# Kernel tuning notes

Measured on AMD Instinct MI355X. Metric: run time of the kernel, lower is better.

## Reference

```python
import jax, jax.numpy as jnp
import numpy as np

B, T, P, L, H = 65536, 256, 4, 14, 32
IN = P + L  # 18


def setup_inputs() -> dict:
    key = jax.random.key(0)
    ks = jax.random.split(key, 8)
    s1 = 1.0 / np.sqrt(IN)
    s2 = 1.0 / np.sqrt(H)
    return {
        "phys": jax.random.normal(ks[0], (B, T, P), dtype=jnp.float32),
        "latents": jax.random.normal(ks[1], (B, L), dtype=jnp.float32),
        "W1": jax.random.uniform(ks[2], (IN, H), jnp.float32, -s1, s1),
        "b1": jax.random.uniform(ks[3], (H,), jnp.float32, -s1, s1),
        "W2": jax.random.uniform(ks[4], (H, H), jnp.float32, -s2, s2),
        "b2": jax.random.uniform(ks[5], (H,), jnp.float32, -s2, s2),
        "W3": jax.random.uniform(ks[6], (H, L), jnp.float32, -s2, s2),
        "b3": jax.random.uniform(ks[7], (L,), jnp.float32, -s2, s2),
    }


def reference(phys, latents, W1, b1, W2, b2, W3, b3):
    # phys: [B, T, P]; latents: [B, L]. Dropout p=0.0 -> identity (eval-equivalent).
    phys_t = jnp.swapaxes(phys, 0, 1)  # [T, B, P] for scan over time

    def step(lat, ph):
        x = jnp.concatenate([ph, lat], axis=1)          # [B, P+L]
        h = jax.nn.relu(x @ W1 + b1)                    # [B, H]
        h = jax.nn.relu(h @ W2 + b2)                    # [B, H]
        lat = lat + (h @ W3 + b3)                       # residual update [B, L]
        return lat, lat

    _, outs = jax.lax.scan(step, latents, phys_t)       # outs: [T, B, L]
    return jnp.swapaxes(outs, 0, 1)                     # [B, T, L]
```

## Files before the change

kernel.cpp:

```cpp
#include <hip/hip_runtime.h>


#define BB 65536
#define TT 256
#define LL 14
#define HH 32

typedef float f32x16 __attribute__((ext_vector_type(16)));
typedef __bf16 bf16x8 __attribute__((ext_vector_type(8)));
typedef __bf16 bf16x2 __attribute__((ext_vector_type(2)));
typedef int i32x2 __attribute__((ext_vector_type(2)));

static __device__ __forceinline__ unsigned packbf(float a, float b) {
    bf16x2 p;
    p[0] = (__bf16)a;
    p[1] = (__bf16)b;
    return __builtin_bit_cast(unsigned, p);
}

static __device__ __forceinline__ void split2(float v0, float v1,
                                              unsigned& hw, unsigned& lw) {
    const __bf16 h0 = (__bf16)v0, h1 = (__bf16)v1;
    hw = packbf(v0, v1);
    const float l0 = v0 - (float)h0;
    const float l1 = v1 - (float)h1;
    lw = packbf(l0, l1);
}

static __device__ __forceinline__ bf16x8 mkfrag(unsigned w0, unsigned w1,
                                                unsigned w2, unsigned w3) {
    union { unsigned u[4]; bf16x8 v; } x;
    x.u[0] = w0; x.u[1] = w1; x.u[2] = w2; x.u[3] = w3;
    return x.v;
}

static __device__ __forceinline__ f32x16 mf(bf16x8 a, bf16x8 b, f32x16 c) {
    return __builtin_amdgcn_mfma_f32_32x32x16_bf16(a, b, c, 0, 0, 0);
}

#if __has_builtin(__builtin_amdgcn_permlane32_swap)
static __device__ __forceinline__ void xswap(unsigned a, unsigned b,
                                             unsigned& a_out, unsigned& b_out) {
    i32x2 r = __builtin_amdgcn_permlane32_swap((int)a, (int)b, false, false);
    a_out = (unsigned)r[0];
    b_out = (unsigned)r[1];
}
#else
static __device__ __forceinline__ void xswap(unsigned a, unsigned b,
                                             unsigned& a_out, unsigned& b_out) {
    const int lane = threadIdx.x & 63;
    const int idx = (lane ^ 32) << 2;
    unsigned sa = (unsigned)__builtin_amdgcn_ds_bpermute(idx, (int)a);
    unsigned sb = (unsigned)__builtin_amdgcn_ds_bpermute(idx, (int)b);
    const bool hi = lane >= 32;
    a_out = hi ? sb : a;
    b_out = hi ? b : sa;
}
#endif

static __device__ __forceinline__ void hfrag(const f32x16& h,
                                             bf16x8& B0h, bf16x8& B0l,
                                             bf16x8& B1h, bf16x8& B1l) {
    unsigned Wh[8], Wl[8];
#pragma unroll
    for (int p = 0; p < 8; ++p) split2(h[2 * p], h[2 * p + 1], Wh[p], Wl[p]);
    unsigned a02h, b02h, a02l, b02l, a13h, b13h, a13l, b13l;
    xswap(Wh[0], Wh[2], a02h, b02h); xswap(Wl[0], Wl[2], a02l, b02l);
    xswap(Wh[1], Wh[3], a13h, b13h); xswap(Wl[1], Wl[3], a13l, b13l);
    B0h = mkfrag(a02h, a13h, b02h, b13h);
    B0l = mkfrag(a02l, a13l, b02l, b13l);
    unsigned a46h, b46h, a46l, b46l, a57h, b57h, a57l, b57l;
    xswap(Wh[4], Wh[6], a46h, b46h); xswap(Wl[4], Wl[6], a46l, b46l);
    xswap(Wh[5], Wh[7], a57h, b57h); xswap(Wl[5], Wl[7], a57l, b57l);
    B1h = mkfrag(a46h, a57h, b46h, b57h);
    B1l = mkfrag(a46l, a57l, b46l, b57l);
}

__global__ __launch_bounds__(256, 2)
void emulator_kernel(const float* __restrict__ phys,
                     const float* __restrict__ latents,
                     const float* __restrict__ W1g,
                     const float* __restrict__ b1g,
                     const float* __restrict__ W2g,
                     const float* __restrict__ b2g,
                     const float* __restrict__ W3g,
                     const float* __restrict__ b3g,
                     float* __restrict__ out) {
    const int tid = threadIdx.x;
    const int lane = tid & 63;
    const int wv = tid >> 6;
    const int c = lane & 31;
    const bool hi = lane >= 32;
    const int kb = hi ? 8 : 0;
    const int r = blockIdx.x * 128 + wv * 32 + c;

    bf16x8 A1t0h, A1t0l, A1c;
    {
        unsigned hw[4], lw[4];
#pragma unroll
        for (int w = 0; w < 4; ++w) {
            const int k0 = kb + 2 * w;
            split2(W1g[k0 * HH + c], W1g[(k0 + 1) * HH + c], hw[w], lw[w]);
        }
        A1t0h = mkfrag(hw[0], hw[1], hw[2], hw[3]);
        A1t0l = mkfrag(lw[0], lw[1], lw[2], lw[3]);
        unsigned whp, wlp;
        split2(W1g[16 * HH + c], W1g[17 * HH + c], whp, wlp);
        A1c = hi ? mkfrag(0, 0, 0, 0) : mkfrag(whp, whp, wlp, 0);
    }
    bf16x8 A2h0, A2l0, A2h1, A2l1, A3h0, A3l0, A3h1, A3l1;
    {
        unsigned hw[4], lw[4];
#pragma unroll
        for (int w = 0; w < 4; ++w) {
            const int k0 = kb + 2 * w;
            split2(W2g[k0 * HH + c], W2g[(k0 + 1) * HH + c], hw[w], lw[w]);
        }
        A2h0 = mkfrag(hw[0], hw[1], hw[2], hw[3]);
        A2l0 = mkfrag(lw[0], lw[1], lw[2], lw[3]);
#pragma unroll
        for (int w = 0; w < 4; ++w) {
            const int k0 = 16 + kb + 2 * w;
            split2(W2g[k0 * HH + c], W2g[(k0 + 1) * HH + c], hw[w], lw[w]);
        }
        A2h1 = mkfrag(hw[0], hw[1], hw[2], hw[3]);
        A2l1 = mkfrag(lw[0], lw[1], lw[2], lw[3]);
#pragma unroll
        for (int w = 0; w < 4; ++w) {
            const int k0 = kb + 2 * w;
            const float e0 = (c < LL) ? W3g[k0 * LL + c] : 0.0f;
            const float e1 = (c < LL) ? W3g[(k0 + 1) * LL + c] : 0.0f;
            split2(e0, e1, hw[w], lw[w]);
        }
        A3h0 = mkfrag(hw[0], hw[1], hw[2], hw[3]);
        A3l0 = mkfrag(lw[0], lw[1], lw[2], lw[3]);
#pragma unroll
        for (int w = 0; w < 4; ++w) {
            const int k0 = 16 + kb + 2 * w;
            const float e0 = (c < LL) ? W3g[k0 * LL + c] : 0.0f;
            const float e1 = (c < LL) ? W3g[(k0 + 1) * LL + c] : 0.0f;
            split2(e0, e1, hw[w], lw[w]);
        }
        A3h1 = mkfrag(hw[0], hw[1], hw[2], hw[3]);
        A3l1 = mkfrag(lw[0], lw[1], lw[2], lw[3]);
    }

    f32x16 cb1, cb2, cb3, z;
#pragma unroll
    for (int rr = 0; rr < 16; ++rr) {
        const int row = (rr & 3) + 8 * (rr >> 2) + (hi ? 4 : 0);
        cb1[rr] = b1g[row];
        cb2[rr] = b2g[row];
        cb3[rr] = (row < LL) ? b3g[row] : 0.0f;
        z[rr] = 0.0f;
    }

    f32x16 lat;
#pragma unroll
    for (int i = 0; i < 16; ++i) lat[i] = 0.0f;
    {
        const float* lrow = latents + (size_t)r * LL;
        const float2* p01 = reinterpret_cast<const float2*>(lrow + (hi ? 4 : 0));
        const float2 v0 = p01[0], v1 = p01[1];
        lat[0] = v0.x; lat[1] = v0.y; lat[2] = v1.x; lat[3] = v1.y;
        const float2 v2 = reinterpret_cast<const float2*>(lrow + (hi ? 12 : 8))[0];
        lat[4] = v2.x; lat[5] = v2.y;
        if (!hi) {
            const float2 v3 = reinterpret_cast<const float2*>(lrow + 10)[0];
            lat[6] = v3.x; lat[7] = v3.y;
        }
    }

    const float4* pv = reinterpret_cast<const float4*>(phys) + (size_t)r * TT;
    float4 ph = pv[0];
    float* outr = out + (size_t)r * TT * LL;

#pragma unroll 1
    for (int t = 0; t < TT; ++t) {
        asm volatile("" : "+v"(A1t0h), "+v"(A1t0l), "+v"(A1c),
                          "+v"(A2h0), "+v"(A2l0), "+v"(A2h1), "+v"(A2l1),
                          "+v"(A3h0), "+v"(A3l0), "+v"(A3h1), "+v"(A3l1),
                          "+v"(cb1), "+v"(cb2), "+v"(cb3), "+v"(z));

        const float4 phn = pv[(t < TT - 1) ? (t + 1) : t];

        unsigned X0h, X0l, X1h, X1l, X2h, X2l, X3h, X3l, P0h, P0l, P1h, P1l;
        split2(lat[0], lat[1], X0h, X0l);
        split2(lat[2], lat[3], X1h, X1l);
        split2(lat[4], lat[5], X2h, X2l);
        split2(lat[6], lat[7], X3h, X3l);
        split2(ph.x, ph.y, P0h, P0l);
        split2(ph.z, ph.w, P1h, P1l);
        unsigned a2h, b2h, a2l, b2l, a3h, b3h, a3l, b3l;
        xswap(X2h, X2h, a2h, b2h); xswap(X2l, X2l, a2l, b2l);
        xswap(X3h, X3h, a3h, b3h); xswap(X3l, X3l, a3l, b3l);
        bf16x8 B0h = mkfrag(hi ? X0h : P0h, hi ? X1h : P1h,
                            hi ? a2h : X0h, hi ? a3h : X1h);
        bf16x8 B0l = mkfrag(hi ? X0l : P0l, hi ? X1l : P1l,
                            hi ? a2l : X0l, hi ? a3l : X1l);
        bf16x8 B1c = mkfrag(b2h, b2l, b2h, 0);

        __builtin_amdgcn_s_setprio(1);
        f32x16 accA = mf(A1t0l, B0h, mf(A1t0h, B0l, mf(A1t0h, B0h, cb1)));
        f32x16 accB = mf(A1c, B1c, z);
        __builtin_amdgcn_s_setprio(0);
        f32x16 h1v;
#pragma unroll
        for (int i = 0; i < 16; ++i) h1v[i] = fmaxf(accA[i] + accB[i], 0.0f);

        bf16x8 C0h, C0l, C1h, C1l;
        hfrag(h1v, C0h, C0l, C1h, C1l);
        __builtin_amdgcn_s_setprio(1);
        f32x16 a2A = mf(A2l0, C0h, mf(A2h0, C0l, mf(A2h0, C0h, cb2)));
        f32x16 a2B = mf(A2l1, C1h, mf(A2h1, C1l, mf(A2h1, C1h, z)));
        __builtin_amdgcn_s_setprio(0);
        f32x16 h2v;
#pragma unroll
        for (int i = 0; i < 16; ++i) h2v[i] = fmaxf(a2A[i] + a2B[i], 0.0f);

        bf16x8 D0h, D0l, D1h, D1l;
        hfrag(h2v, D0h, D0l, D1h, D1l);
        f32x16 c3;
#pragma unroll
        for (int i = 0; i < 16; ++i) c3[i] = lat[i] + cb3[i];
        __builtin_amdgcn_s_setprio(1);
        f32x16 nlA = mf(A3l0, D0h, mf(A3h0, D0l, mf(A3h0, D0h, c3)));
        f32x16 nlB = mf(A3l1, D1h, mf(A3h1, D1l, mf(A3h1, D1h, z)));
        __builtin_amdgcn_s_setprio(0);
#pragma unroll
        for (int i = 0; i < 16; ++i) lat[i] = nlA[i] + nlB[i];

        float* ob = outr + (size_t)t * LL;
        const int o0 = hi ? 4 : 0;
        *reinterpret_cast<float2*>(ob + o0)     = make_float2(lat[0], lat[1]);
        *reinterpret_cast<float2*>(ob + o0 + 2) = make_float2(lat[2], lat[3]);
        *reinterpret_cast<float2*>(ob + (hi ? 12 : 8)) = make_float2(lat[4], lat[5]);
        if (!hi)
            *reinterpret_cast<float2*>(ob + 10) = make_float2(lat[6], lat[7]);

        ph = phn;
    }
}

extern "C" void kernel_launch(void* const* d_in, const int* in_sizes, int n_in,
                              void* d_out, int out_size, void* d_ws, size_t ws_size,
                              hipStream_t stream) {
    const float* phys    = (const float*)d_in[0];
    const float* latents = (const float*)d_in[1];
    const float* W1      = (const float*)d_in[2];
    const float* b1      = (const float*)d_in[3];
    const float* W2      = (const float*)d_in[4];
    const float* b2      = (const float*)d_in[5];
    const float* W3      = (const float*)d_in[6];
    const float* b3      = (const float*)d_in[7];
    float* out = (float*)d_out;

    const int threads = 256;
    const int blocks = BB / 128;
    emulator_kernel<<<blocks, threads, 0, stream>>>(
        phys, latents, W1, b1, W2, b2, W3, b3, out);
}
```

Baseline: 600.4 us.

## Stage output latents in LDS and flush eight timesteps as float4 stores

```diff
diff --git a/kernel.cpp b/kernel.cpp
--- a/kernel.cpp
+++ b/kernel.cpp
@@ -5,6 +5,7 @@
 #define TT 256
 #define LL 14
 #define HH 32
+#define RSTRIDE 116
 
 typedef float f32x16 __attribute__((ext_vector_type(16)));
 typedef __bf16 bf16x8 __attribute__((ext_vector_type(8)));
@@ -86,6 +87,8 @@
                      const float* __restrict__ W3g,
                      const float* __restrict__ b3g,
                      float* __restrict__ out) {
+    __shared__ float lds[4 * 32 * RSTRIDE];
+
     const int tid = threadIdx.x;
     const int lane = tid & 63;
     const int wv = tid >> 6;
@@ -174,6 +177,11 @@
     const float4* pv = reinterpret_cast<const float4*>(phys) + (size_t)r * TT;
     float4 ph = pv[0];
     float* outr = out + (size_t)r * TT * LL;
+
+    float* wrow_base = lds + wv * 32 * RSTRIDE + c * RSTRIDE;
+    const int halfsel = hi ? 1 : 0;
+    const float4* fl_src = reinterpret_cast<const float4*>(
+        lds + wv * 32 * RSTRIDE + c * RSTRIDE + halfsel * 56);
 
 #pragma unroll 1
     for (int t = 0; t < TT; ++t) {
@@ -220,23 +228,33 @@
 
         bf16x8 D0h, D0l, D1h, D1l;
         hfrag(h2v, D0h, D0l, D1h, D1l);
-        f32x16 c3;
-#pragma unroll
-        for (int i = 0; i < 16; ++i) c3[i] = lat[i] + cb3[i];
         __builtin_amdgcn_s_setprio(1);
-        f32x16 nlA = mf(A3l0, D0h, mf(A3h0, D0l, mf(A3h0, D0h, c3)));
-        f32x16 nlB = mf(A3l1, D1h, mf(A3h1, D1l, mf(A3h1, D1h, z)));
+        f32x16 nlA = mf(A3l0, D0h, mf(A3h0, D0l, mf(A3h0, D0h, lat)));
+        f32x16 nlB = mf(A3l1, D1h, mf(A3h1, D1l, mf(A3h1, D1h, cb3)));
         __builtin_amdgcn_s_setprio(0);
 #pragma unroll
-        for (int i = 0; i < 16; ++i) lat[i] = nlA[i] + nlB[i];
-
-        float* ob = outr + (size_t)t * LL;
-        const int o0 = hi ? 4 : 0;
-        *reinterpret_cast<float2*>(ob + o0)     = make_float2(lat[0], lat[1]);
-        *reinterpret_cast<float2*>(ob + o0 + 2) = make_float2(lat[2], lat[3]);
-        *reinterpret_cast<float2*>(ob + (hi ? 12 : 8)) = make_float2(lat[4], lat[5]);
-        if (!hi)
-            *reinterpret_cast<float2*>(ob + 10) = make_float2(lat[6], lat[7]);
+        for (int i = 0; i < 8; ++i) lat[i] = nlA[i] + nlB[i];
+
+        {
+            float* wr = wrow_base + (t & 7) * LL;
+            if (!hi) {
+                *reinterpret_cast<float2*>(wr + 0)  = make_float2(lat[0], lat[1]);
+                *reinterpret_cast<float2*>(wr + 2)  = make_float2(lat[2], lat[3]);
+                *reinterpret_cast<float2*>(wr + 8)  = make_float2(lat[4], lat[5]);
+                *reinterpret_cast<float2*>(wr + 10) = make_float2(lat[6], lat[7]);
+            } else {
+                *reinterpret_cast<float2*>(wr + 4)  = make_float2(lat[0], lat[1]);
+                *reinterpret_cast<float2*>(wr + 6)  = make_float2(lat[2], lat[3]);
+                *reinterpret_cast<float2*>(wr + 12) = make_float2(lat[4], lat[5]);
+            }
+        }
+
+        if ((t & 7) == 7) {
+            float4* gdst = reinterpret_cast<float4*>(
+                outr + (size_t)(t - 7 + 4 * halfsel) * LL);
+#pragma unroll
+            for (int q = 0; q < 14; ++q) gdst[q] = fl_src[q];
+        }
 
         ph = phn;
     }
```

After: 593.2 us. About the same (-1.2%).
